# Kernel tuning notes

Measured on AMD Instinct MI355X. Metric: run time of the kernel, lower is better.

The kernel has to match this reference:

```python
import jax, jax.numpy as jnp
import numpy as np

D = 256       # d_model
HEADS = 8     # n_heads
PTS = 4       # n_points
FF = 1024     # dim_feedforward
HD = D // HEADS
B, Q = 8, 900
HH, WW = 100, 100


def setup_inputs() -> dict:
    key = jax.random.key(0)
    ks = iter(jax.random.split(key, 40))
    p = lambda shape: jax.random.normal(next(ks), shape, dtype=jnp.float32) * 0.02
    inp = {
        "tgt": jax.random.normal(next(ks), (B, Q, D), dtype=jnp.float32),
        "memory": jax.random.normal(next(ks), (B, HH * WW, D), dtype=jnp.float32),
        "H": HH,
        "W": WW,
        # self-attention (nn.MultiheadAttention) params
        "in_proj_w": p((3 * D, D)), "in_proj_b": p((3 * D,)),
        "out_proj_w": p((D, D)), "out_proj_b": p((D,)),
        # layer norms
        "norm1_s": jnp.ones((D,)), "norm1_b": jnp.zeros((D,)),
        "norm2_s": jnp.ones((D,)), "norm2_b": jnp.zeros((D,)),
        "norm3_s": jnp.ones((D,)), "norm3_b": jnp.zeros((D,)),
        # deformable cross-attention params
        "vproj_w": p((D, D)), "vproj_b": p((D,)),
        "offs_w": p((HEADS * PTS * 2, D)), "offs_b": p((HEADS * PTS * 2,)),
        "attw_w": p((HEADS * PTS, D)), "attw_b": p((HEADS * PTS,)),
        "ref_w": p((2, D)), "ref_b": p((2,)),
        "cout_w": p((D, D)), "cout_b": p((D,)),
        # FFN params
        "ffn_w1": p((FF, D)), "ffn_b1": p((FF,)),
        "ffn_w2": p((D, FF)), "ffn_b2": p((D,)),
    }
    return inp


def _layer_norm(x, s, b):
    m = jnp.mean(x, -1, keepdims=True)
    v = jnp.mean((x - m) ** 2, -1, keepdims=True)
    return (x - m) * jax.lax.rsqrt(v + 1e-5) * s + b


def _mha(x, wi, bi, wo, bo):
    b, q, _ = x.shape
    qkv = x @ wi.T + bi
    qh, kh, vh = jnp.split(qkv, 3, axis=-1)
    qh = qh.reshape(b, q, HEADS, HD).transpose(0, 2, 1, 3)
    kh = kh.reshape(b, q, HEADS, HD).transpose(0, 2, 1, 3)
    vh = vh.reshape(b, q, HEADS, HD).transpose(0, 2, 1, 3)
    att = jax.nn.softmax(jnp.einsum('bhqd,bhkd->bhqk', qh, kh) / np.float32(np.sqrt(HD)), axis=-1)
    o = jnp.einsum('bhqk,bhkd->bhqd', att, vh).transpose(0, 2, 1, 3).reshape(b, q, D)
    return o @ wo.T + bo


def _deform_attn(q, mem, H, W, vproj_w, vproj_b, offs_w, offs_b, attw_w, attw_b,
                 ref_w, ref_b, cout_w, cout_b):
    b, nq, _ = q.shape
    # per-query normalized reference points (x, y) in [0,1]
    ref = jax.nn.sigmoid(q @ ref_w.T + ref_b)                         # [B,Q,2]
    offs = (q @ offs_w.T + offs_b).reshape(b, nq, HEADS, PTS, 2)      # [B,Q,h,p,2]
    attw = jax.nn.softmax((q @ attw_w.T + attw_b).reshape(b, nq, HEADS, PTS), axis=-1)
    val = (mem @ vproj_w.T + vproj_b).reshape(b, H * W, HEADS, HD).transpose(0, 2, 1, 3)  # [B,h,HW,hd]
    wh = jnp.array([W, H], dtype=q.dtype)
    loc = ref[:, :, None, None, :] + offs / wh                        # normalized sampling loc
    x = loc[..., 0] * W - 0.5                                         # pixel coords (align_corners=False)
    y = loc[..., 1] * H - 0.5
    x0 = jnp.floor(x); y0 = jnp.floor(y)
    lx = x - x0; ly = y - y0
    x0i = x0.astype(jnp.int32); y0i = y0.astype(jnp.int32)

    def gather(xi, yi):
        valid = ((xi >= 0) & (xi < W) & (yi >= 0) & (yi < H)).astype(q.dtype)
        idx = jnp.clip(yi, 0, H - 1) * W + jnp.clip(xi, 0, W - 1)     # [B,Q,h,p]
        idxt = idx.transpose(0, 2, 1, 3).reshape(b, HEADS, nq * PTS, 1)
        g = jnp.take_along_axis(val, idxt, axis=2)                    # [B,h,Q*p,hd]
        g = g.reshape(b, HEADS, nq, PTS, HD).transpose(0, 2, 1, 3, 4)  # [B,Q,h,p,hd]
        return g * valid[..., None]

    samp = (gather(x0i, y0i) * ((1 - lx) * (1 - ly))[..., None]
            + gather(x0i + 1, y0i) * (lx * (1 - ly))[..., None]
            + gather(x0i, y0i + 1) * ((1 - lx) * ly)[..., None]
            + gather(x0i + 1, y0i + 1) * (lx * ly)[..., None])        # [B,Q,h,p,hd]
    out = jnp.sum(samp * attw[..., None], axis=3).reshape(b, nq, D)
    return out @ cout_w.T + cout_b


def reference(tgt, memory, H, W, in_proj_w, in_proj_b, out_proj_w, out_proj_b,
              norm1_s, norm1_b, norm2_s, norm2_b, norm3_s, norm3_b,
              vproj_w, vproj_b, offs_w, offs_b, attw_w, attw_b, ref_w, ref_b,
              cout_w, cout_b, ffn_w1, ffn_b1, ffn_w2, ffn_b2):
    t2 = _mha(tgt, in_proj_w, in_proj_b, out_proj_w, out_proj_b)
    t = _layer_norm(tgt + t2, norm1_s, norm1_b)
    t2 = _deform_attn(t, memory, H, W, vproj_w, vproj_b, offs_w, offs_b,
                      attw_w, attw_b, ref_w, ref_b, cout_w, cout_b)
    t = _layer_norm(t + t2, norm2_s, norm2_b)
    f = jnp.maximum(t @ ffn_w1.T + ffn_b1, 0) @ ffn_w2.T + ffn_b2
    return _layer_norm(t + f, norm3_s, norm3_b)
```

## Files before the change

### kernel.cpp

```cpp
#include <hip/hip_runtime.h>
#include <hip/hip_bf16.h>

typedef __hip_bfloat16 bf16;
typedef __attribute__((ext_vector_type(8))) short short8;
typedef __attribute__((ext_vector_type(4))) float f32x4;

#define BB 8
#define QQ 900
#define DD 256
#define NH 8
#define HD 32
#define NPTS 4
#define FFD 1024
#define HH 100
#define WW2 100
#define HWTOT 10000

#define QT 64
#define KTC 128
#define NCHUNK ((QQ + KTC - 1) / KTC)
#define QB 4

__device__ inline float tofloat(float x) { return x; }
__device__ inline float tofloat(bf16 x) { return __bfloat162float(x); }
__device__ inline float bf2f(unsigned short u) {
    return __uint_as_float(((unsigned int)u) << 16);
}
__device__ inline void storev(bf16* p, float v) { *p = __float2bfloat16(v); }
__device__ inline void storev(float* p, float v) { *p = v; }

typedef __attribute__((address_space(1))) const unsigned int gas_u32;
typedef __attribute__((address_space(3))) unsigned int las_u32;
__device__ inline void gload_lds16(const bf16* g, bf16* l) {
    __builtin_amdgcn_global_load_lds(
        (gas_u32*)(unsigned long long)(const void*)g,
        (las_u32*)(unsigned int)(unsigned long long)(const void*)l, 16, 0, 0);
}

__global__ void pack_kernel(const float* __restrict__ in_proj_w, const float* __restrict__ out_proj_w,
                            const float* __restrict__ cout_w, const float* __restrict__ ffn_w1,
                            const float* __restrict__ ffn_w2, const float* __restrict__ vproj_w,
                            const float* __restrict__ offs_w, const float* __restrict__ attw_w,
                            const float* __restrict__ ref_w, const float* __restrict__ offs_b,
                            const float* __restrict__ attw_b, const float* __restrict__ ref_b,
                            const float* __restrict__ tgt, bf16* __restrict__ wpk,
                            bf16* __restrict__ tgtb, float* __restrict__ dbias) {
    const int idx = blockIdx.x * 256 + threadIdx.x;
    const int TOT = 950272 + 1843200 + 128;
    if (idx >= TOT) return;
    if (idx < 196608) {
        wpk[idx] = __float2bfloat16(in_proj_w[idx]);
    } else if (idx < 262144) {
        wpk[idx] = __float2bfloat16(out_proj_w[idx - 196608]);
    } else if (idx < 327680) {
        wpk[idx] = __float2bfloat16(cout_w[idx - 262144]);
    } else if (idx < 589824) {
        wpk[idx] = __float2bfloat16(ffn_w1[idx - 327680]);
    } else if (idx < 851968) {
        wpk[idx] = __float2bfloat16(ffn_w2[idx - 589824]);
    } else if (idx < 917504) {
        wpk[idx] = __float2bfloat16(vproj_w[idx - 851968]);
    } else if (idx < 950272) {
        const int j = idx - 917504;
        const int r = j >> 8, c = j & 255;
        float v = 0.f;
        if (r < 64) v = offs_w[r * 256 + c];
        else if (r < 96) v = attw_w[(r - 64) * 256 + c];
        else if (r < 98) v = ref_w[(r - 96) * 256 + c];
        wpk[idx] = __float2bfloat16(v);
    } else if (idx < 950272 + 1843200) {
        const int j = idx - 950272;
        tgtb[j] = __float2bfloat16(tgt[j]);
    } else {
        const int j = idx - (950272 + 1843200);
        float v = 0.f;
        if (j < 64) v = offs_b[j];
        else if (j < 96) v = attw_b[j - 64];
        else if (j < 98) v = ref_b[j - 96];
        dbias[j] = v;
    }
}

template <int BN, int ACT, typename OT>
__global__ __launch_bounds__(256) void gemm_mfma_kernel(const bf16* __restrict__ A,
                                                        const bf16* __restrict__ W,
                                                        const float* __restrict__ bias,
                                                        OT* __restrict__ C, int M, int N, int K) {
    constexpr int WC = BN / 2;
    constexpr int NACC = WC / 16;
    __shared__ bf16 As[128 * 32];
    __shared__ bf16 Bs[BN * 32];
    const int bm = blockIdx.y * 128, bn = blockIdx.x * BN;
    const int tid = threadIdx.x;
    const int lane = tid & 63, wave = tid >> 6;
    const int l15 = lane & 15, g = lane >> 4;
    const int wr = wave >> 1, wc = wave & 1;
    const int lrow = lane >> 2, lcol = (lane & 3) * 8;
    const f32x4 zf = {0.f, 0.f, 0.f, 0.f};
    f32x4 acc[4][NACC];
#pragma unroll
    for (int mi = 0; mi < 4; ++mi)
#pragma unroll
        for (int ni = 0; ni < NACC; ++ni) acc[mi][ni] = zf;

    for (int k0 = 0; k0 < K; k0 += 32) {
        __syncthreads();
#pragma unroll
        for (int i = 0; i < 2; ++i) {
            const int chunk = wave * 2 + i;
            const int arow = min(bm + chunk * 16 + lrow, M - 1);
            gload_lds16(A + (size_t)arow * K + k0 + lcol, &As[chunk * 512]);
        }
#pragma unroll
        for (int i = 0; i < BN / 64; ++i) {
            const int chunk = wave * (BN / 64) + i;
            gload_lds16(W + (size_t)(bn + chunk * 16 + lrow) * K + k0 + lcol, &Bs[chunk * 512]);
        }
        __syncthreads();
        short8 af[4];
#pragma unroll
        for (int mi = 0; mi < 4; ++mi)
            af[mi] = *(const short8*)&As[(wr * 64 + mi * 16 + l15) * 32 + g * 8];
#pragma unroll
        for (int ni = 0; ni < NACC; ++ni) {
            const short8 bfv = *(const short8*)&Bs[(wc * WC + ni * 16 + l15) * 32 + g * 8];
#pragma unroll
            for (int mi = 0; mi < 4; ++mi)
                acc[mi][ni] =
                    __builtin_amdgcn_mfma_f32_16x16x32_bf16(af[mi], bfv, acc[mi][ni], 0, 0, 0);
        }
    }
#pragma unroll
    for (int ni = 0; ni < NACC; ++ni) {
        const int col = bn + wc * WC + ni * 16 + l15;
        const float bv = bias[col];
#pragma unroll
        for (int mi = 0; mi < 4; ++mi) {
#pragma unroll
            for (int r = 0; r < 4; ++r) {
                const int row = bm + wr * 64 + mi * 16 + g * 4 + r;
                if (row < M) {
                    float v = acc[mi][ni][r] + bv;
                    if (ACT == 1) v = fmaxf(v, 0.f);
                    storev(&C[(size_t)row * N + col], v);
                }
            }
        }
    }
}

__global__ __launch_bounds__(256) void mha_mfma_kernel(const bf16* __restrict__ qkv,
                                                       bf16* __restrict__ o) {
    const int qt = blockIdx.x, h = blockIdx.y, b = blockIdx.z;
    const int tid = threadIdx.x;
    const int lane = tid & 63, wave = tid >> 6;
    const int l15 = lane & 15, g = lane >> 4;
    __shared__ unsigned short Kls[KTC][40];
    __shared__ bf16 Vt[HD][136];
    __shared__ bf16 Pls[4][16][136];
    const size_t base = (size_t)b * QQ * 768;
    const int q0 = qt * QT;

    short8 qa = {0, 0, 0, 0, 0, 0, 0, 0};
    {
        const int qg = q0 + wave * 16 + l15;
        if (qg < QQ)
            qa = *(const short8*)(qkv + base + (size_t)qg * 768 + h * HD + g * 8);
    }
    f32x4 accO[2] = {{0.f, 0.f, 0.f, 0.f}, {0.f, 0.f, 0.f, 0.f}};
    float m_run[4], l_run[4];
#pragma unroll
    for (int r = 0; r < 4; ++r) {
        m_run[r] = -1e30f;
        l_run[r] = 0.f;
    }
    const float scale = 0.17677669529663687f;
    const uint4 zero4 = {0u, 0u, 0u, 0u};

    for (int c = 0; c < NCHUNK; ++c) {
        const int k0 = c * KTC;
        __syncthreads();
        {
            const int part = tid & 3, kr = tid >> 2;
#pragma unroll
            for (int pass = 0; pass < 2; ++pass) {
                const int krr = kr + pass * 64;
                const int kg = k0 + krr;
                uint4 kv = (kg < QQ)
                    ? *(const uint4*)(qkv + base + (size_t)kg * 768 + DD + h * HD + part * 8)
                    : zero4;
                *(uint4*)&Kls[krr][part * 8] = kv;
            }
        }
        {
            const int kr = tid >> 1, ch0 = (tid & 1) * 16;
            const int kg = k0 + kr;
            uint4 v0 = zero4, v1 = zero4;
            if (kg < QQ) {
                const bf16* pv = qkv + base + (size_t)kg * 768 + 2 * DD + h * HD + ch0;
                v0 = *(const uint4*)pv;
                v1 = *(const uint4*)(pv + 8);
            }
            const unsigned short* u0 = (const unsigned short*)&v0;
            const unsigned short* u1 = (const unsigned short*)&v1;
#pragma unroll
            for (int j = 0; j < 8; ++j) {
                ((unsigned short*)&Vt[ch0 + j][kr])[0] = u0[j];
                ((unsigned short*)&Vt[ch0 + 8 + j][kr])[0] = u1[j];
            }
        }
        __syncthreads();

        f32x4 s[8];
#pragma unroll
        for (int t = 0; t < 8; ++t) {
            const short8 kb = *(const short8*)&Kls[t * 16 + l15][g * 8];
            const f32x4 z = {0.f, 0.f, 0.f, 0.f};
            s[t] = __builtin_amdgcn_mfma_f32_16x16x32_bf16(qa, kb, z, 0, 0, 0);
        }
        float mx[4] = {-1e30f, -1e30f, -1e30f, -1e30f};
#pragma unroll
        for (int t = 0; t < 8; ++t) {
            const bool cv = (k0 + t * 16 + l15) < QQ;
#pragma unroll
            for (int r = 0; r < 4; ++r) {
                const float v = cv ? s[t][r] * scale : -1e30f;
                s[t][r] = v;
                mx[r] = fmaxf(mx[r], v);
            }
        }
#pragma unroll
        for (int r = 0; r < 4; ++r) {
            mx[r] = fmaxf(mx[r], __shfl_xor(mx[r], 1));
            mx[r] = fmaxf(mx[r], __shfl_xor(mx[r], 2));
            mx[r] = fmaxf(mx[r], __shfl_xor(mx[r], 4));
            mx[r] = fmaxf(mx[r], __shfl_xor(mx[r], 8));
        }
        float alpha[4], rs[4];
#pragma unroll
        for (int r = 0; r < 4; ++r) {
            const float mn = fmaxf(m_run[r], mx[r]);
            alpha[r] = __expf(m_run[r] - mn);
            m_run[r] = mn;
            rs[r] = 0.f;
        }
#pragma unroll
        for (int t = 0; t < 8; ++t) {
#pragma unroll
            for (int r = 0; r < 4; ++r) {
                const float p = __expf(s[t][r] - m_run[r]);
                rs[r] += p;
                Pls[wave][g * 4 + r][t * 16 + l15] = __float2bfloat16(p);
            }
        }
#pragma unroll
        for (int r = 0; r < 4; ++r) {
            rs[r] += __shfl_xor(rs[r], 1);
            rs[r] += __shfl_xor(rs[r], 2);
            rs[r] += __shfl_xor(rs[r], 4);
            rs[r] += __shfl_xor(rs[r], 8);
            l_run[r] = l_run[r] * alpha[r] + rs[r];
        }
#pragma unroll
        for (int t2 = 0; t2 < 2; ++t2)
#pragma unroll
            for (int r = 0; r < 4; ++r) accO[t2][r] *= alpha[r];
#pragma unroll
        for (int s4 = 0; s4 < 4; ++s4) {
            const short8 pa = *(const short8*)&Pls[wave][l15][s4 * 32 + g * 8];
#pragma unroll
            for (int t2 = 0; t2 < 2; ++t2) {
                const short8 vb = *(const short8*)&Vt[t2 * 16 + l15][s4 * 32 + g * 8];
                accO[t2] = __builtin_amdgcn_mfma_f32_16x16x32_bf16(pa, vb, accO[t2], 0, 0, 0);
            }
        }
    }
#pragma unroll
    for (int r = 0; r < 4; ++r) {
        const int row = q0 + wave * 16 + g * 4 + r;
        if (row < QQ) {
            const float inv = 1.f / l_run[r];
#pragma unroll
            for (int t2 = 0; t2 < 2; ++t2) {
                storev(&o[((size_t)b * QQ + row) * DD + h * HD + t2 * 16 + l15],
                       accO[t2][r] * inv);
            }
        }
    }
}

template <typename TR, typename TO>
__global__ void add_ln_kernel(const TR* __restrict__ resid, const bf16* __restrict__ y,
                              const float* __restrict__ g, const float* __restrict__ bta,
                              TO* __restrict__ out) {
    const int row = blockIdx.x;
    const int tid = threadIdx.x;
    const int lane = tid & 63, wave = tid >> 6;
    __shared__ float red[4];
    const size_t idx = (size_t)row * DD + tid;
    float v = tofloat(resid[idx]) + tofloat(y[idx]);
    float s = v;
    s += __shfl_xor(s, 1);  s += __shfl_xor(s, 2);  s += __shfl_xor(s, 4);
    s += __shfl_xor(s, 8);  s += __shfl_xor(s, 16); s += __shfl_xor(s, 32);
    if (lane == 0) red[wave] = s;
    __syncthreads();
    const float mean = (red[0] + red[1] + red[2] + red[3]) * (1.f / DD);
    const float d = v - mean;
    float q = d * d;
    q += __shfl_xor(q, 1);  q += __shfl_xor(q, 2);  q += __shfl_xor(q, 4);
    q += __shfl_xor(q, 8);  q += __shfl_xor(q, 16); q += __shfl_xor(q, 32);
    __syncthreads();
    if (lane == 0) red[wave] = q;
    __syncthreads();
    const float rstd = rsqrtf((red[0] + red[1] + red[2] + red[3]) * (1.f / DD) + 1e-5f);
    storev(&out[idx], d * rstd * g[tid] + bta[tid]);
}

__global__ __launch_bounds__(256) void deform_gather_kernel(
    const float* __restrict__ dots, const float* __restrict__ mem,
    bf16* __restrict__ G, float* __restrict__ wsumg) {
    const int qt = blockIdx.x, b = blockIdx.y;
    const int tid = threadIdx.x;
    const int q0 = qt * QB;
    __shared__ int sidx[QB][32][4];
    __shared__ float swt[QB][32][4];

    if (tid < 128) {
        const int q = tid >> 5, hp = tid & 31;
        const float* dr = dots + ((size_t)b * QQ + q0 + q) * 128;
        const float ox = dr[hp * 2], oy = dr[hp * 2 + 1];
        float ad = dr[64 + hp];
        const float rx = dr[96], ry = dr[97];
        float mx = ad;
        mx = fmaxf(mx, __shfl_xor(mx, 1));
        mx = fmaxf(mx, __shfl_xor(mx, 2));
        float e = __expf(ad - mx);
        float sm = e;
        sm += __shfl_xor(sm, 1);
        sm += __shfl_xor(sm, 2);
        const float a = e / sm;
        const float refx = 1.f / (1.f + __expf(-rx));
        const float refy = 1.f / (1.f + __expf(-ry));
        const float x = (refx + ox * (1.f / WW2)) * WW2 - 0.5f;
        const float y = (refy + oy * (1.f / HH)) * HH - 0.5f;
        const float x0f = floorf(x), y0f = floorf(y);
        const float lx = x - x0f, ly = y - y0f;
        const int x0 = (int)x0f, y0 = (int)y0f;
        const float cw[4] = {(1 - lx) * (1 - ly), lx * (1 - ly), (1 - lx) * ly, lx * ly};
        const int cx[4] = {x0, x0 + 1, x0, x0 + 1};
        const int cy[4] = {y0, y0, y0 + 1, y0 + 1};
        float cs = 0.f;
#pragma unroll
        for (int cc = 0; cc < 4; ++cc) {
            const bool valid = cx[cc] >= 0 && cx[cc] < WW2 && cy[cc] >= 0 && cy[cc] < HH;
            const int xi = min(max(cx[cc], 0), WW2 - 1);
            const int yi = min(max(cy[cc], 0), HH - 1);
            sidx[q][hp][cc] = yi * WW2 + xi;
            const float w = valid ? a * cw[cc] : 0.f;
            swt[q][hp][cc] = w;
            cs += w;
        }
        cs += __shfl_xor(cs, 1);
        cs += __shfl_xor(cs, 2);
        if ((hp & 3) == 0) wsumg[((size_t)b * QQ + q0 + q) * NH + (hp >> 2)] = cs;
    }
    __syncthreads();

    {
        const int q = tid >> 6, cbase = (tid & 63) * 4;
        const float* mb = mem + (size_t)b * HWTOT * DD;
        bf16* gq = G + ((size_t)(b * QQ + q0 + q) * NH) * DD + cbase;
#pragma unroll
        for (int h = 0; h < NH; ++h) {
            float4 acc = {0.f, 0.f, 0.f, 0.f};
#pragma unroll
            for (int p = 0; p < NPTS; ++p) {
                const int hp = h * NPTS + p;
                const int4 ix = *(const int4*)sidx[q][hp];
                const float4 wt = *(const float4*)swt[q][hp];
                const float4 v0 = *(const float4*)(mb + (size_t)ix.x * DD + cbase);
                const float4 v1 = *(const float4*)(mb + (size_t)ix.y * DD + cbase);
                const float4 v2 = *(const float4*)(mb + (size_t)ix.z * DD + cbase);
                const float4 v3 = *(const float4*)(mb + (size_t)ix.w * DD + cbase);
                acc.x += wt.x * v0.x + wt.y * v1.x + wt.z * v2.x + wt.w * v3.x;
                acc.y += wt.x * v0.y + wt.y * v1.y + wt.z * v2.y + wt.w * v3.y;
                acc.z += wt.x * v0.z + wt.y * v1.z + wt.z * v2.z + wt.w * v3.z;
                acc.w += wt.x * v0.w + wt.y * v1.w + wt.z * v2.w + wt.w * v3.w;
            }
            bf16 out4[4] = {__float2bfloat16(acc.x), __float2bfloat16(acc.y),
                            __float2bfloat16(acc.z), __float2bfloat16(acc.w)};
            *(uint2*)(gq + (size_t)h * DD) = *(const uint2*)out4;
        }
    }
}

__global__ __launch_bounds__(256) void gemm_vproj_kernel(
    const bf16* __restrict__ G, const bf16* __restrict__ Wv,
    const float* __restrict__ vb, const float* __restrict__ wsumg,
    bf16* __restrict__ samp, int M) {
    __shared__ unsigned short As[64][40];
    __shared__ unsigned short Bs[32][40];
    const int h = blockIdx.x, bm = blockIdx.y * 64;
    const int tid = threadIdx.x;
    const int lane = tid & 63, wave = tid >> 6;
    const int l15 = lane & 15, g = lane >> 4;
    const int sr = tid >> 2, sc = (tid & 3) * 8;
    f32x4 acc[2] = {{0.f, 0.f, 0.f, 0.f}, {0.f, 0.f, 0.f, 0.f}};
    const uint4 zero4 = {0u, 0u, 0u, 0u};
    for (int k0 = 0; k0 < DD; k0 += 32) {
        __syncthreads();
        {
            const int arow = bm + sr;
            uint4 a4 = (arow < M)
                ? *(const uint4*)(G + ((size_t)arow * NH + h) * DD + k0 + sc)
                : zero4;
            *(uint4*)&As[sr][sc] = a4;
            if (sr < 32) {
                uint4 b4 = *(const uint4*)(Wv + (size_t)(h * 32 + sr) * DD + k0 + sc);
                *(uint4*)&Bs[sr][sc] = b4;
            }
        }
        __syncthreads();
        const short8 af = *(const short8*)&As[wave * 16 + l15][g * 8];
#pragma unroll
        for (int ct = 0; ct < 2; ++ct) {
            const short8 bf = *(const short8*)&Bs[ct * 16 + l15][g * 8];
            acc[ct] = __builtin_amdgcn_mfma_f32_16x16x32_bf16(af, bf, acc[ct], 0, 0, 0);
        }
    }
#pragma unroll
    for (int ct = 0; ct < 2; ++ct) {
        const int col = h * 32 + ct * 16 + l15;
        const float bv = vb[col];
#pragma unroll
        for (int r = 0; r < 4; ++r) {
            const int row = bm + wave * 16 + g * 4 + r;
            if (row < M) {
                const float v = acc[ct][r] + bv * wsumg[(size_t)row * NH + h];
                storev(&samp[(size_t)row * DD + col], v);
            }
        }
    }
}

extern "C" void kernel_launch(void* const* d_in, const int* in_sizes, int n_in,
                              void* d_out, int out_size, void* d_ws, size_t ws_size,
                              hipStream_t stream) {
    const float* tgt = (const float*)d_in[0];
    const float* memory = (const float*)d_in[1];
    const float* in_proj_w = (const float*)d_in[4];
    const float* in_proj_b = (const float*)d_in[5];
    const float* out_proj_w = (const float*)d_in[6];
    const float* out_proj_b = (const float*)d_in[7];
    const float* norm1_s = (const float*)d_in[8];
    const float* norm1_b = (const float*)d_in[9];
    const float* norm2_s = (const float*)d_in[10];
    const float* norm2_b = (const float*)d_in[11];
    const float* norm3_s = (const float*)d_in[12];
    const float* norm3_b = (const float*)d_in[13];
    const float* vproj_w = (const float*)d_in[14];
    const float* vproj_b = (const float*)d_in[15];
    const float* offs_w = (const float*)d_in[16];
    const float* offs_b = (const float*)d_in[17];
    const float* attw_w = (const float*)d_in[18];
    const float* attw_b = (const float*)d_in[19];
    const float* ref_w = (const float*)d_in[20];
    const float* ref_b = (const float*)d_in[21];
    const float* cout_w = (const float*)d_in[22];
    const float* cout_b = (const float*)d_in[23];
    const float* ffn_w1 = (const float*)d_in[24];
    const float* ffn_b1 = (const float*)d_in[25];
    const float* ffn_w2 = (const float*)d_in[26];
    const float* ffn_b2 = (const float*)d_in[27];

    const int M = BB * QQ;
    bf16* ws = (bf16*)d_ws;
    size_t off = 0;
    bf16* qkv = ws + off;  off += (size_t)M * 768;
    bf16* o = ws + off;    off += (size_t)M * DD;
    bf16* t1 = ws + off;   off += (size_t)M * DD;
    bf16* tmp = ws + off;  off += (size_t)M * DD;
    bf16* ffh = ws + off;  off += (size_t)M * FFD;
    bf16* tgtb = ws + off; off += (size_t)M * DD;
    bf16* wpk = ws + off;  off += 950272;
    float* dbias = (float*)(ws + off); off += 256;
    float* wsumg = (float*)(ws + off); off += (size_t)M * NH * 2;
    bf16* Gws = ws + off;  off += (size_t)M * NH * DD;
    bf16* samp = o;
    bf16* t2n = qkv;
    float* dots = (float*)ffh;

    bf16* w_in = wpk;
    bf16* w_out = wpk + 196608;
    bf16* w_cout = wpk + 262144;
    bf16* w_ffn1 = wpk + 327680;
    bf16* w_ffn2 = wpk + 589824;
    bf16* w_vproj = wpk + 851968;
    bf16* w_dots = wpk + 917504;

    const int MT = (M + 63) / 64;
    const int MT2 = (M + 127) / 128;

    pack_kernel<<<(950272 + 1843200 + 128 + 255) / 256, 256, 0, stream>>>(
        in_proj_w, out_proj_w, cout_w, ffn_w1, ffn_w2, vproj_w, offs_w, attw_w, ref_w,
        offs_b, attw_b, ref_b, tgt, wpk, tgtb, dbias);
    gemm_mfma_kernel<128, 0, bf16><<<dim3(6, MT2), 256, 0, stream>>>(tgtb, w_in, in_proj_b,
                                                                     qkv, M, 768, DD);
    mha_mfma_kernel<<<dim3((QQ + QT - 1) / QT, NH, BB), 256, 0, stream>>>(qkv, o);
    gemm_mfma_kernel<64, 0, bf16><<<dim3(4, MT2), 256, 0, stream>>>(o, w_out, out_proj_b,
                                                                    tmp, M, DD, DD);
    add_ln_kernel<float, bf16><<<M, 256, 0, stream>>>(tgt, tmp, norm1_s, norm1_b, t1);
    gemm_mfma_kernel<64, 0, float><<<dim3(2, MT2), 256, 0, stream>>>(t1, w_dots, dbias,
                                                                     dots, M, 128, DD);
    deform_gather_kernel<<<dim3(QQ / QB, BB), 256, 0, stream>>>(dots, memory, Gws, wsumg);
    gemm_vproj_kernel<<<dim3(NH, MT), 256, 0, stream>>>(Gws, w_vproj, vproj_b, wsumg,
                                                        samp, M);
    gemm_mfma_kernel<64, 0, bf16><<<dim3(4, MT2), 256, 0, stream>>>(samp, w_cout, cout_b,
                                                                    tmp, M, DD, DD);
    add_ln_kernel<bf16, bf16><<<M, 256, 0, stream>>>(t1, tmp, norm2_s, norm2_b, t2n);
    gemm_mfma_kernel<128, 1, bf16><<<dim3(8, MT2), 256, 0, stream>>>(t2n, w_ffn1, ffn_b1,
                                                                     ffh, M, FFD, DD);
    gemm_mfma_kernel<64, 0, bf16><<<dim3(4, MT2), 256, 0, stream>>>(ffh, w_ffn2, ffn_b2,
                                                                    tmp, M, DD, FFD);
    add_ln_kernel<bf16, float><<<M, 256, 0, stream>>>(t2n, tmp, norm3_s, norm3_b,
                                                      (float*)d_out);
}
```

Baseline: 370.1 us.

## Double-buffer swizzled GEMM tiles and emit transposed V for attention

```diff
diff --git a/kernel.cpp b/kernel.cpp
--- a/kernel.cpp
+++ b/kernel.cpp
@@ -20,6 +20,7 @@
 #define KTC 128
 #define NCHUNK ((QQ + KTC - 1) / KTC)
 #define QB 4
+#define VTP 1024
 
 __device__ inline float tofloat(float x) { return x; }
 __device__ inline float tofloat(bf16 x) { return __bfloat162float(x); }
@@ -44,9 +45,10 @@
                             const float* __restrict__ ref_w, const float* __restrict__ offs_b,
                             const float* __restrict__ attw_b, const float* __restrict__ ref_b,
                             const float* __restrict__ tgt, bf16* __restrict__ wpk,
-                            bf16* __restrict__ tgtb, float* __restrict__ dbias) {
+                            bf16* __restrict__ tgtb, float* __restrict__ dbias,
+                            bf16* __restrict__ vt) {
     const int idx = blockIdx.x * 256 + threadIdx.x;
-    const int TOT = 950272 + 1843200 + 128;
+    const int TOT = 950272 + 1843200 + 128 + 2097152;
     if (idx >= TOT) return;
     if (idx < 196608) {
         wpk[idx] = __float2bfloat16(in_proj_w[idx]);
@@ -71,101 +73,143 @@
     } else if (idx < 950272 + 1843200) {
         const int j = idx - 950272;
         tgtb[j] = __float2bfloat16(tgt[j]);
-    } else {
+    } else if (idx < 950272 + 1843200 + 128) {
         const int j = idx - (950272 + 1843200);
         float v = 0.f;
         if (j < 64) v = offs_b[j];
         else if (j < 96) v = attw_b[j - 64];
         else if (j < 98) v = ref_b[j - 96];
         dbias[j] = v;
-    }
-}
-
-template <int BN, int ACT, typename OT>
-__global__ __launch_bounds__(256) void gemm_mfma_kernel(const bf16* __restrict__ A,
-                                                        const bf16* __restrict__ W,
-                                                        const float* __restrict__ bias,
-                                                        OT* __restrict__ C, int M, int N, int K) {
-    constexpr int WC = BN / 2;
-    constexpr int NACC = WC / 16;
-    __shared__ bf16 As[128 * 32];
-    __shared__ bf16 Bs[BN * 32];
-    const int bm = blockIdx.y * 128, bn = blockIdx.x * BN;
+    } else {
+        vt[idx - (950272 + 1843200 + 128)] = __float2bfloat16(0.f);
+    }
+}
+
+template <int BN, int ACT, int VT, typename OT>
+__global__ __launch_bounds__(256) void gemm_v3(const bf16* __restrict__ A,
+                                               const bf16* __restrict__ W,
+                                               const float* __restrict__ bias,
+                                               OT* __restrict__ C, bf16* __restrict__ vt,
+                                               int M, int N, int K) {
+    constexpr int NACC = BN / 32;
+    __shared__ bf16 As[2][64 * 32];
+    __shared__ bf16 Bs[2][BN * 32];
+    const int bm = blockIdx.y * 64, bn = blockIdx.x * BN;
     const int tid = threadIdx.x;
     const int lane = tid & 63, wave = tid >> 6;
     const int l15 = lane & 15, g = lane >> 4;
-    const int wr = wave >> 1, wc = wave & 1;
-    const int lrow = lane >> 2, lcol = (lane & 3) * 8;
+    const int wr = wave & 1, wc = wave >> 1;
     const f32x4 zf = {0.f, 0.f, 0.f, 0.f};
-    f32x4 acc[4][NACC];
-#pragma unroll
-    for (int mi = 0; mi < 4; ++mi)
+    f32x4 acc[2][NACC];
+#pragma unroll
+    for (int mi = 0; mi < 2; ++mi)
 #pragma unroll
         for (int ni = 0; ni < NACC; ++ni) acc[mi][ni] = zf;
 
-    for (int k0 = 0; k0 < K; k0 += 32) {
-        __syncthreads();
-#pragma unroll
-        for (int i = 0; i < 2; ++i) {
-            const int chunk = wave * 2 + i;
-            const int arow = min(bm + chunk * 16 + lrow, M - 1);
-            gload_lds16(A + (size_t)arow * K + k0 + lcol, &As[chunk * 512]);
-        }
+    const int s_row = wave * 16 + (lane >> 2);
+    const int s_p = lane & 3;
+    const int s_agp = s_p ^ ((s_row >> 1) & 3);
+    const int a_grow = min(bm + s_row, M - 1);
+
+    const int NT = K / 32;
+    int cur = 0;
+
+    {
+        gload_lds16(A + (size_t)a_grow * K + 0 + s_agp * 8, &As[0][wave * 512]);
 #pragma unroll
         for (int i = 0; i < BN / 64; ++i) {
-            const int chunk = wave * (BN / 64) + i;
-            gload_lds16(W + (size_t)(bn + chunk * 16 + lrow) * K + k0 + lcol, &Bs[chunk * 512]);
-        }
-        __syncthreads();
-        short8 af[4];
-#pragma unroll
-        for (int mi = 0; mi < 4; ++mi)
-            af[mi] = *(const short8*)&As[(wr * 64 + mi * 16 + l15) * 32 + g * 8];
+            const int r = (wave * (BN / 64) + i) * 16 + (lane >> 2);
+            const int gp = s_p ^ ((r >> 1) & 3);
+            gload_lds16(W + (size_t)(bn + r) * K + 0 + gp * 8, &Bs[0][(wave * (BN / 64) + i) * 512]);
+        }
+    }
+    __syncthreads();
+
+    for (int t = 0; t < NT; ++t) {
+        if (t + 1 < NT) {
+            const int k0 = (t + 1) * 32;
+            gload_lds16(A + (size_t)a_grow * K + k0 + s_agp * 8, &As[cur ^ 1][wave * 512]);
+#pragma unroll
+            for (int i = 0; i < BN / 64; ++i) {
+                const int r = (wave * (BN / 64) + i) * 16 + (lane >> 2);
+                const int gp = s_p ^ ((r >> 1) & 3);
+                gload_lds16(W + (size_t)(bn + r) * K + k0 + gp * 8,
+                            &Bs[cur ^ 1][(wave * (BN / 64) + i) * 512]);
+            }
+        }
+        short8 af[2];
+#pragma unroll
+        for (int mi = 0; mi < 2; ++mi) {
+            const int row = wr * 32 + mi * 16 + l15;
+            af[mi] = *(const short8*)&As[cur][row * 32 + (g ^ ((row >> 1) & 3)) * 8];
+        }
 #pragma unroll
         for (int ni = 0; ni < NACC; ++ni) {
-            const short8 bfv = *(const short8*)&Bs[(wc * WC + ni * 16 + l15) * 32 + g * 8];
-#pragma unroll
-            for (int mi = 0; mi < 4; ++mi)
+            const int col = wc * (BN / 2) + ni * 16 + l15;
+            const short8 bfv = *(const short8*)&Bs[cur][col * 32 + (g ^ ((col >> 1) & 3)) * 8];
+#pragma unroll
+            for (int mi = 0; mi < 2; ++mi)
                 acc[mi][ni] =
                     __builtin_amdgcn_mfma_f32_16x16x32_bf16(af[mi], bfv, acc[mi][ni], 0, 0, 0);
         }
-    }
+        __syncthreads();
+        cur ^= 1;
+    }
+
 #pragma unroll
     for (int ni = 0; ni < NACC; ++ni) {
-        const int col = bn + wc * WC + ni * 16 + l15;
+        const int col = bn + wc * (BN / 2) + ni * 16 + l15;
         const float bv = bias[col];
 #pragma unroll
-        for (int mi = 0; mi < 4; ++mi) {
-#pragma unroll
-            for (int r = 0; r < 4; ++r) {
-                const int row = bm + wr * 64 + mi * 16 + g * 4 + r;
-                if (row < M) {
-                    float v = acc[mi][ni][r] + bv;
-                    if (ACT == 1) v = fmaxf(v, 0.f);
-                    storev(&C[(size_t)row * N + col], v);
+        for (int mi = 0; mi < 2; ++mi) {
+            const int row0 = bm + wr * 32 + mi * 16 + g * 4;
+            if (VT && col >= 512) {
+                if (row0 < M) {
+                    const int b = row0 / 900, q = row0 % 900;
+                    const int hd = col - 512;
+                    bf16 u4[4];
+#pragma unroll
+                    for (int r = 0; r < 4; ++r) u4[r] = __float2bfloat16(acc[mi][ni][r] + bv);
+                    *(uint2*)&vt[((size_t)(b * NH + (hd >> 5)) * HD + (hd & 31)) * VTP + q] =
+                        *(const uint2*)u4;
                 }
+            } else {
+#pragma unroll
+                for (int r = 0; r < 4; ++r) {
+                    const int row = row0 + r;
+                    if (row < M) {
+                        float v = acc[mi][ni][r] + bv;
+                        if (ACT == 1) v = fmaxf(v, 0.f);
+                        if (VT)
+                            storev((bf16*)C + (size_t)row * 512 + col, v);
+                        else
+                            storev(&C[(size_t)row * N + col], v);
+                    }
+                }
             }
         }
     }
 }
 
 __global__ __launch_bounds__(256) void mha_mfma_kernel(const bf16* __restrict__ qkv,
+                                                       const bf16* __restrict__ vt,
                                                        bf16* __restrict__ o) {
     const int qt = blockIdx.x, h = blockIdx.y, b = blockIdx.z;
     const int tid = threadIdx.x;
     const int lane = tid & 63, wave = tid >> 6;
     const int l15 = lane & 15, g = lane >> 4;
-    __shared__ unsigned short Kls[KTC][40];
-    __shared__ bf16 Vt[HD][136];
-    __shared__ bf16 Pls[4][16][136];
-    const size_t base = (size_t)b * QQ * 768;
+    __shared__ bf16 KP[8704];
+    __shared__ bf16 Vls[4096];
+    bf16(*Pls)[16][136] = (bf16(*)[16][136])KP;
+    const size_t base = (size_t)b * QQ * 512;
+    const bf16* vbase = vt + (size_t)(b * NH + h) * HD * VTP;
     const int q0 = qt * QT;
 
     short8 qa = {0, 0, 0, 0, 0, 0, 0, 0};
     {
         const int qg = q0 + wave * 16 + l15;
         if (qg < QQ)
-            qa = *(const short8*)(qkv + base + (size_t)qg * 768 + h * HD + g * 8);
+            qa = *(const short8*)(qkv + base + (size_t)qg * 512 + h * HD + g * 8);
     }
     f32x4 accO[2] = {{0.f, 0.f, 0.f, 0.f}, {0.f, 0.f, 0.f, 0.f}};
     float m_run[4], l_run[4];
@@ -175,46 +219,33 @@
         l_run[r] = 0.f;
     }
     const float scale = 0.17677669529663687f;
-    const uint4 zero4 = {0u, 0u, 0u, 0u};
 
     for (int c = 0; c < NCHUNK; ++c) {
         const int k0 = c * KTC;
         __syncthreads();
-        {
-            const int part = tid & 3, kr = tid >> 2;
-#pragma unroll
-            for (int pass = 0; pass < 2; ++pass) {
-                const int krr = kr + pass * 64;
-                const int kg = k0 + krr;
-                uint4 kv = (kg < QQ)
-                    ? *(const uint4*)(qkv + base + (size_t)kg * 768 + DD + h * HD + part * 8)
-                    : zero4;
-                *(uint4*)&Kls[krr][part * 8] = kv;
-            }
-        }
-        {
-            const int kr = tid >> 1, ch0 = (tid & 1) * 16;
-            const int kg = k0 + kr;
-            uint4 v0 = zero4, v1 = zero4;
-            if (kg < QQ) {
-                const bf16* pv = qkv + base + (size_t)kg * 768 + 2 * DD + h * HD + ch0;
-                v0 = *(const uint4*)pv;
-                v1 = *(const uint4*)(pv + 8);
-            }
-            const unsigned short* u0 = (const unsigned short*)&v0;
-            const unsigned short* u1 = (const unsigned short*)&v1;
-#pragma unroll
-            for (int j = 0; j < 8; ++j) {
-                ((unsigned short*)&Vt[ch0 + j][kr])[0] = u0[j];
-                ((unsigned short*)&Vt[ch0 + 8 + j][kr])[0] = u1[j];
-            }
+#pragma unroll
+        for (int i = 0; i < 2; ++i) {
+            const int r = (wave * 2 + i) * 16 + (lane >> 2);
+            const int p = lane & 3;
+            const int gp = p ^ ((r >> 1) & 3);
+            const int kg = min(k0 + r, QQ - 1);
+            gload_lds16(qkv + base + (size_t)kg * 512 + 256 + h * HD + gp * 8,
+                        &KP[(wave * 2 + i) * 512]);
+        }
+#pragma unroll
+        for (int i = 0; i < 2; ++i) {
+            const int s = (wave * 2 + i) * 64 + lane;
+            const int vrow = s >> 4, vp = s & 15;
+            const int gp = vp ^ (vrow & 7);
+            gload_lds16(vbase + (size_t)vrow * VTP + k0 + gp * 8, &Vls[(wave * 2 + i) * 512]);
         }
         __syncthreads();
 
         f32x4 s[8];
 #pragma unroll
         for (int t = 0; t < 8; ++t) {
-            const short8 kb = *(const short8*)&Kls[t * 16 + l15][g * 8];
+            const int row = t * 16 + l15;
+            const short8 kb = *(const short8*)&KP[row * 32 + (g ^ ((row >> 1) & 3)) * 8];
             const f32x4 z = {0.f, 0.f, 0.f, 0.f};
             s[t] = __builtin_amdgcn_mfma_f32_16x16x32_bf16(qa, kb, z, 0, 0, 0);
         }
@@ -244,6 +275,7 @@
             m_run[r] = mn;
             rs[r] = 0.f;
         }
+        __syncthreads();
 #pragma unroll
         for (int t = 0; t < 8; ++t) {
 #pragma unroll
@@ -270,7 +302,9 @@
             const short8 pa = *(const short8*)&Pls[wave][l15][s4 * 32 + g * 8];
 #pragma unroll
             for (int t2 = 0; t2 < 2; ++t2) {
-                const short8 vb = *(const short8*)&Vt[t2 * 16 + l15][s4 * 32 + g * 8];
+                const int vrow = t2 * 16 + l15;
+                const int pp = (s4 * 4 + g) ^ (vrow & 7);
+                const short8 vb = *(const short8*)&Vls[vrow * 128 + pp * 8];
                 accO[t2] = __builtin_amdgcn_mfma_f32_16x16x32_bf16(pa, vb, accO[t2], 0, 0, 0);
             }
         }
@@ -476,7 +510,7 @@
     const int M = BB * QQ;
     bf16* ws = (bf16*)d_ws;
     size_t off = 0;
-    bf16* qkv = ws + off;  off += (size_t)M * 768;
+    bf16* qkv = ws + off;  off += (size_t)M * 512;
     bf16* o = ws + off;    off += (size_t)M * DD;
     bf16* t1 = ws + off;   off += (size_t)M * DD;
     bf16* tmp = ws + off;  off += (size_t)M * DD;
@@ -486,6 +520,7 @@
     float* dbias = (float*)(ws + off); off += 256;
     float* wsumg = (float*)(ws + off); off += (size_t)M * NH * 2;
     bf16* Gws = ws + off;  off += (size_t)M * NH * DD;
+    bf16* vt = ws + off;   off += (size_t)BB * NH * HD * VTP;
     bf16* samp = o;
     bf16* t2n = qkv;
     float* dots = (float*)ffh;
@@ -499,29 +534,28 @@
     bf16* w_dots = wpk + 917504;
 
     const int MT = (M + 63) / 64;
-    const int MT2 = (M + 127) / 128;
-
-    pack_kernel<<<(950272 + 1843200 + 128 + 255) / 256, 256, 0, stream>>>(
+
+    pack_kernel<<<(950272 + 1843200 + 128 + 2097152 + 255) / 256, 256, 0, stream>>>(
         in_proj_w, out_proj_w, cout_w, ffn_w1, ffn_w2, vproj_w, offs_w, attw_w, ref_w,
-        offs_b, attw_b, ref_b, tgt, wpk, tgtb, dbias);
-    gemm_mfma_kernel<128, 0, bf16><<<dim3(6, MT2), 256, 0, stream>>>(tgtb, w_in, in_proj_b,
-                                                                     qkv, M, 768, DD);
-    mha_mfma_kernel<<<dim3((QQ + QT - 1) / QT, NH, BB), 256, 0, stream>>>(qkv, o);
-    gemm_mfma_kernel<64, 0, bf16><<<dim3(4, MT2), 256, 0, stream>>>(o, w_out, out_proj_b,
-                                                                    tmp, M, DD, DD);
+        offs_b, attw_b, ref_b, tgt, wpk, tgtb, dbias, vt);
+    gemm_v3<128, 0, 1, bf16><<<dim3(6, MT), 256, 0, stream>>>(tgtb, w_in, in_proj_b,
+                                                              qkv, vt, M, 768, DD);
+    mha_mfma_kernel<<<dim3((QQ + QT - 1) / QT, NH, BB), 256, 0, stream>>>(qkv, vt, o);
+    gemm_v3<64, 0, 0, bf16><<<dim3(4, MT), 256, 0, stream>>>(o, w_out, out_proj_b,
+                                                             tmp, nullptr, M, DD, DD);
     add_ln_kernel<float, bf16><<<M, 256, 0, stream>>>(tgt, tmp, norm1_s, norm1_b, t1);
-    gemm_mfma_kernel<64, 0, float><<<dim3(2, MT2), 256, 0, stream>>>(t1, w_dots, dbias,
-                                                                     dots, M, 128, DD);
+    gemm_v3<64, 0, 0, float><<<dim3(2, MT), 256, 0, stream>>>(t1, w_dots, dbias,
+                                                              dots, nullptr, M, 128, DD);
     deform_gather_kernel<<<dim3(QQ / QB, BB), 256, 0, stream>>>(dots, memory, Gws, wsumg);
     gemm_vproj_kernel<<<dim3(NH, MT), 256, 0, stream>>>(Gws, w_vproj, vproj_b, wsumg,
                                                         samp, M);
-    gemm_mfma_kernel<64, 0, bf16><<<dim3(4, MT2), 256, 0, stream>>>(samp, w_cout, cout_b,
-                                                                    tmp, M, DD, DD);
+    gemm_v3<64, 0, 0, bf16><<<dim3(4, MT), 256, 0, stream>>>(samp, w_cout, cout_b,
+                                                             tmp, nullptr, M, DD, DD);
     add_ln_kernel<bf16, bf16><<<M, 256, 0, stream>>>(t1, tmp, norm2_s, norm2_b, t2n);
-    gemm_mfma_kernel<128, 1, bf16><<<dim3(8, MT2), 256, 0, stream>>>(t2n, w_ffn1, ffn_b1,
-                                                                     ffh, M, FFD, DD);
-    gemm_mfma_kernel<64, 0, bf16><<<dim3(4, MT2), 256, 0, stream>>>(ffh, w_ffn2, ffn_b2,
-                                                                    tmp, M, DD, FFD);
+    gemm_v3<128, 1, 0, bf16><<<dim3(8, MT), 256, 0, stream>>>(t2n, w_ffn1, ffn_b1,
+                                                              ffh, nullptr, M, FFD, DD);
+    gemm_v3<64, 0, 0, bf16><<<dim3(4, MT), 256, 0, stream>>>(ffh, w_ffn2, ffn_b2,
+                                                             tmp, nullptr, M, DD, FFD);
     add_ln_kernel<bf16, float><<<M, 256, 0, stream>>>(t2n, tmp, norm3_s, norm3_b,
                                                       (float*)d_out);
 }
```

Result: faster. 345.9 us (-6.5%).
